# Kernel tuning notes

Hardware: AMD Instinct MI355X
Metric: run time of the kernel (lower is better)

## Reference

```python
import jax, jax.numpy as jnp
import numpy as np

B = 256                       # graphs in batch
NS = [4096, 2048, 1024, 512]  # nodes per graph at each stage (pool halves)
F_IN = 3                      # num_feature
D = 64                        # dim_cell
EPB = [32768, 16384, 8192]    # edges per graph at each layer (deg ~8)
NEG = 0.2                     # GATConv leaky_relu negative slope
EPS = 1e-5                    # BatchNorm eps
L = 3                         # layer_cell


def setup_inputs() -> dict:
    key = jax.random.key(0)
    ks = jax.random.split(key, 16)
    inp = {"x": jax.random.normal(ks[0], (B * NS[0], F_IN), jnp.float32)}
    dims = [F_IN, D, D]
    for i in range(L):
        inp[f"W{i}"] = jax.random.normal(ks[1 + i], (dims[i], D), jnp.float32) / np.sqrt(dims[i]).astype(np.float32)
        inp[f"as{i}"] = jax.random.normal(ks[4 + i], (D,), jnp.float32) * 0.1
        inp[f"ad{i}"] = jax.random.normal(ks[7 + i], (D,), jnp.float32) * 0.1
        inp[f"b{i}"] = jnp.zeros((D,), jnp.float32)
        inp[f"e{i}"] = jax.random.randint(ks[10 + i], (2, EPB[i]), 0, NS[i], jnp.int32)
        # cluster assignment: merge node pairs -> every cluster id occupied
        inp[f"c{i}"] = (jnp.arange(NS[i], dtype=jnp.int32) // 2)
    return inp


def _tile_edges(edge, n_per_graph):
    # replicate per-graph edge list across batch with node offsets, then add self-loops
    offs = (jnp.arange(B, dtype=edge.dtype) * n_per_graph)
    e = (edge[:, None, :] + offs[None, :, None]).reshape(2, -1)  # [2, B*E]
    loops = jnp.arange(B * n_per_graph, dtype=edge.dtype)
    return jnp.concatenate([e, jnp.stack([loops, loops])], axis=1)


def _gat(x, W, a_src, a_dst, bias, edge, n_tot):
    # PyG GATConv, heads=1: shared linear, edge-softmax over incoming edges
    h = x @ W                                # [n_tot, D]
    al_s = h @ a_src                         # [n_tot]
    al_d = h @ a_dst
    src, dst = edge[0], edge[1]              # message src j -> target i
    e = jax.nn.leaky_relu(al_s[src] + al_d[dst], NEG)
    m = jax.ops.segment_max(e, dst, num_segments=n_tot)
    ex = jnp.exp(e - m[dst])
    z = jax.ops.segment_sum(ex, dst, num_segments=n_tot)
    alpha = ex / z[dst]                      # softmax per target node
    out = jax.ops.segment_sum(alpha[:, None] * h[src], dst, num_segments=n_tot)
    return out + bias


def reference(x, W0, as0, ad0, b0, W1, as1, ad1, b1, W2, as2, ad2, b2,
              e0, e1, e2, c0, c1, c2):
    Ws, As, Ad, Bs = [W0, W1, W2], [as0, as1, as2], [ad0, ad1, ad2], [b0, b1, b2]
    Es, Cs = [e0, e1, e2], [c0, c1, c2]
    h = x
    for i in range(L):
        n_tot = B * NS[i]
        edge = _tile_edges(Es[i], NS[i])
        h = jax.nn.relu(_gat(h, Ws[i], As[i], Ad[i], Bs[i], edge, n_tot))
        # cluster max_pool: scatter-max nodes into clusters, offset per graph
        c_out = NS[i + 1]
        seg = (Cs[i][None, :] + (jnp.arange(B, dtype=jnp.int32) * c_out)[:, None]).reshape(-1)
        h = jax.ops.segment_max(h, seg, num_segments=B * c_out)
        # BatchNorm1d(affine=False), training-mode batch statistics
        h = (h - h.mean(axis=0)) * jax.lax.rsqrt(h.var(axis=0) + EPS)
    return h.reshape(B, NS[L] * D)
```

## Files before the change

### kernel.cpp

```cpp
#include <hip/hip_runtime.h>
#include <stdint.h>

#define NEG_SLOPE 0.2f
#define BN_EPS 1e-5f

typedef unsigned short u16;
typedef unsigned int   u32;
typedef __attribute__((ext_vector_type(2))) float  v2f;
typedef __attribute__((ext_vector_type(4))) float  f32x4;
typedef __attribute__((ext_vector_type(8))) short  short8;

__device__ __forceinline__ float lrelu(float x){ return fmaxf(x, NEG_SLOPE*x); }
__device__ __forceinline__ float bf2f(u16 u){ return __uint_as_float(((u32)u) << 16); }
__device__ __forceinline__ u16 f2bf(float f){
  u32 u = __float_as_uint(f);
  return (u16)((u + 0x7fffu + ((u >> 16) & 1u)) >> 16);
}

__global__ __launch_bounds__(256) void init_k(int* __restrict__ counts, u32* __restrict__ s0,
                                              u32* __restrict__ s1, u32* __restrict__ s2,
                                              int nc, int n0, int n1, int n2){
  int t = blockIdx.x*256 + threadIdx.x;
  int y = blockIdx.y;
  if (y==0){ if (t<nc) counts[t]=0; }
  else {
    u32* sd = (y==1)?s0:(y==2)?s1:s2;
    int n   = (y==1)?n0:(y==2)?n1:n2;
    if (t<n) sd[t]=0xFFFFFFFFu;
  }
}

__global__ __launch_bounds__(256) void hist_all_k(const int* __restrict__ el0, const int* __restrict__ el1,
                                                  const int* __restrict__ el2, int* __restrict__ c0,
                                                  int* __restrict__ c1, int* __restrict__ c2,
                                                  int n0, int n1, int n2){
  int t = blockIdx.x*256 + threadIdx.x;
  int L = blockIdx.y;
  const int* dst = (L==0)?(el0+n0):(L==1)?(el1+n1):(el2+n2);
  int* counts    = (L==0)?c0:(L==1)?c1:c2;
  int n          = (L==0)?n0:(L==1)?n1:n2;
  if (t < n) atomicAdd(&counts[dst[t]], 1);
}

__global__ __launch_bounds__(1024) void scan_all_k(int* __restrict__ c0, int* __restrict__ c1, int* __restrict__ c2,
                         int* __restrict__ ip0, int* __restrict__ ip1, int* __restrict__ ip2,
                         int* __restrict__ cu0, int* __restrict__ cu1, int* __restrict__ cu2,
                         u32* __restrict__ sd0, u32* __restrict__ sd1, u32* __restrict__ sd2,
                         int n0, int n1, int n2){
  int L = blockIdx.x;
  const int* counts = (L==0)?c0:(L==1)?c1:c2;
  int* indptr2      = (L==0)?ip0:(L==1)?ip1:ip2;
  int* cursor       = (L==0)?cu0:(L==1)?cu1:cu2;
  u32* sd           = (L==0)?sd0:(L==1)?sd1:sd2;
  int n             = (L==0)?n0:(L==1)?n1:n2;
  __shared__ int part[1024];
  int tid = threadIdx.x;
  int base = tid*4;
  int v0=0,v1=0,v2=0,v3=0;
  if (base+0<n) v0 = (counts[base+0]+4)&~3;
  if (base+1<n) v1 = (counts[base+1]+4)&~3;
  if (base+2<n) v2 = (counts[base+2]+4)&~3;
  if (base+3<n) v3 = (counts[base+3]+4)&~3;
  part[tid] = v0+v1+v2+v3;
  __syncthreads();
  for (int off=1; off<1024; off<<=1){
    int t2 = (tid>=off)?part[tid-off]:0;
    __syncthreads();
    part[tid] += t2;
    __syncthreads();
  }
  int run = (tid>0)?part[tid-1]:0;
  if (base+0<n){ indptr2[base+0]=run; cursor[base+0]=run+1; sd[run]=(u32)(base+0)|((u32)(base+0)<<16); run+=v0; }
  if (base+1<n){ indptr2[base+1]=run; cursor[base+1]=run+1; sd[run]=(u32)(base+1)|((u32)(base+1)<<16); run+=v1; }
  if (base+2<n){ indptr2[base+2]=run; cursor[base+2]=run+1; sd[run]=(u32)(base+2)|((u32)(base+2)<<16); run+=v2; }
  if (base+3<n){ indptr2[base+3]=run; cursor[base+3]=run+1; sd[run]=(u32)(base+3)|((u32)(base+3)<<16); run+=v3; }
  if (tid==0) indptr2[n] = part[1023];
}

__global__ __launch_bounds__(256) void scatter_all_k(const int* __restrict__ el0, const int* __restrict__ el1,
                         const int* __restrict__ el2, int* __restrict__ cu0, int* __restrict__ cu1,
                         int* __restrict__ cu2, u32* __restrict__ sd0, u32* __restrict__ sd1,
                         u32* __restrict__ sd2, int n0, int n1, int n2){
  int t = blockIdx.x*256 + threadIdx.x;
  int L = blockIdx.y;
  const int* el = (L==0)?el0:(L==1)?el1:el2;
  int* cursor   = (L==0)?cu0:(L==1)?cu1:cu2;
  u32* sd       = (L==0)?sd0:(L==1)?sd1:sd2;
  int n         = (L==0)?n0:(L==1)?n1:n2;
  if (t < n){
    int dd = el[n + t];
    int p = atomicAdd(&cursor[dd], 1);
    sd[p] = (u32)el[t] | ((u32)dd << 16);
  }
}

__global__ __launch_bounds__(1024) void pairsort_k(const int* __restrict__ c0, const int* __restrict__ c1,
                         const int* __restrict__ c2, u16* __restrict__ pm0, u16* __restrict__ pm1,
                         u16* __restrict__ pm2, int np0, int np1, int np2){
  int L = blockIdx.x;
  const int* counts = (L==0)?c0:(L==1)?c1:c2;
  u16* perm = (L==0)?pm0:(L==1)?pm1:pm2;
  int np    = (L==0)?np0:(L==1)?np1:np2;
  __shared__ int hist[64];
  __shared__ int pos[64];
  int t = threadIdx.x;
  if (t < 64) hist[t] = 0;
  __syncthreads();
  for (int p=t; p<np; p+=1024){
    int k = min(max(counts[2*p], counts[2*p+1]), 63);
    atomicAdd(&hist[k], 1);
  }
  __syncthreads();
  if (t == 0){ int run=0; for (int i=0;i<64;i++){ pos[i]=run; run+=hist[i]; } }
  __syncthreads();
  for (int p=t; p<np; p+=1024){
    int k = min(max(counts[2*p], counts[2*p+1]), 63);
    int q = atomicAdd(&pos[k], 1);
    perm[q] = (u16)p;
  }
}

__global__ __launch_bounds__(256) void gemm3_k(const float* __restrict__ x, const float* __restrict__ Wg,
                        const float* __restrict__ asrc, const float* __restrict__ adst,
                        u16* __restrict__ h, float* __restrict__ als, float* __restrict__ ald, int nrows8)
{
  const int l = threadIdx.x & 63;
  const int g = l >> 3;
  const int o = l & 7;
  float W0[8], W1[8], W2[8];
  float vs0=0.f,vs1=0.f,vs2=0.f,vd0=0.f,vd1=0.f,vd2=0.f;
  #pragma unroll
  for (int j=0;j<8;j++){
    W0[j] = Wg[      o*8 + j];
    W1[j] = Wg[ 64 + o*8 + j];
    W2[j] = Wg[128 + o*8 + j];
    float as = asrc[o*8 + j], ad = adst[o*8 + j];
    vs0 = fmaf(W0[j], as, vs0); vs1 = fmaf(W1[j], as, vs1); vs2 = fmaf(W2[j], as, vs2);
    vd0 = fmaf(W0[j], ad, vd0); vd1 = fmaf(W1[j], ad, vd1); vd2 = fmaf(W2[j], ad, vd2);
  }
  #pragma unroll
  for (int off=1; off<8; off<<=1){
    vs0 += __shfl_xor(vs0,off); vs1 += __shfl_xor(vs1,off); vs2 += __shfl_xor(vs2,off);
    vd0 += __shfl_xor(vd0,off); vd1 += __shfl_xor(vd1,off); vd2 += __shfl_xor(vd2,off);
  }
  int wv = blockIdx.x*4 + (int)(threadIdx.x>>6);
  int stride = gridDim.x*4;
  for (int blk = wv; blk < nrows8; blk += stride){
    int r = blk*8 + g;
    float x0 = x[(size_t)r*3+0];
    float x1 = x[(size_t)r*3+1];
    float x2 = x[(size_t)r*3+2];
    u32 pk[4];
    #pragma unroll
    for (int j=0;j<8;j+=2){
      float a0 = fmaf(x0, W0[j],   fmaf(x1, W1[j],   x2*W2[j]));
      float a1 = fmaf(x0, W0[j+1], fmaf(x1, W1[j+1], x2*W2[j+1]));
      pk[j>>1] = (u32)f2bf(a0) | ((u32)f2bf(a1) << 16);
    }
    ((int4*)(h + ((size_t)r << 6)))[o] = make_int4((int)pk[0],(int)pk[1],(int)pk[2],(int)pk[3]);
    if (o == 0){
      als[r] = fmaf(x2, vs2, fmaf(x1, vs1, x0*vs0));
      ald[r] = fmaf(x2, vd2, fmaf(x1, vd1, x0*vd0));
    }
  }
}

__global__ __launch_bounds__(128) void prep_w_k(const float* __restrict__ W, const float* __restrict__ asrc,
                        const float* __restrict__ adst, const float* __restrict__ scratch, float invN,
                        u16* __restrict__ wswz, float* __restrict__ cvec){
  __shared__ float mean_s[64], rstd_s[64], vs_s[64], vd_s[64], cv_s[64], acc[128];
  int t = threadIdx.x;
  float s = 0.f;
  #pragma unroll 8
  for (int b2=0;b2<256;b2++) s += scratch[b2*128 + t];
  acc[t] = s;
  __syncthreads();
  if (t < 64){
    float m = acc[t]*invN;
    float var = acc[64+t]*invN - m*m;
    mean_s[t] = m; rstd_s[t] = rsqrtf(var + BN_EPS);
  }
  __syncthreads();
  if (t < 64){
    float c = 0.f;
    for (int k=0;k<64;k++) c = fmaf(mean_s[k]*rstd_s[k], W[k*64+t], c);
    cv_s[t] = c; cvec[t] = c;
    float vs = 0.f, vd = 0.f;
    for (int col=0; col<64; col++){
      float wv = W[t*64+col];
      vs = fmaf(wv, asrc[col], vs);
      vd = fmaf(wv, adst[col], vd);
    }
    vs_s[t] = rstd_s[t]*vs; vd_s[t] = rstd_s[t]*vd;
  }
  __syncthreads();
  if (t == 0){
    float cs=0.f, cd=0.f;
    for (int col=0; col<64; col++){ cs = fmaf(cv_s[col], asrc[col], cs); cd = fmaf(cv_s[col], adst[col], cd); }
    cvec[64] = cs; cvec[65] = cd;
  }
  if (t < 64){
    #pragma unroll
    for (int f=0; f<8; f++){
      int tt = f >> 1, ch = f & 1;
      #pragma unroll
      for (int j=0; j<8; j++){
        int k   = ch*32 + (t>>4)*8 + j;
        int col = tt*16 + (t&15);
        wswz[(f*64 + t)*8 + j] = f2bf(rstd_s[k] * W[k*64 + col]);
      }
    }
    #pragma unroll
    for (int f=8; f<10; f++){
      int ch = f - 8;
      #pragma unroll
      for (int j=0; j<8; j++){
        int k = ch*32 + (t>>4)*8 + j;
        int colp = t & 15;
        float val = (colp==0)? vs_s[k] : (colp==1)? vd_s[k] : 0.f;
        wswz[(f*64 + t)*8 + j] = f2bf(val);
      }
    }
  }
}

__global__ __launch_bounds__(256) void gemm64_mfma_k(const u16* __restrict__ Pin, const u16* __restrict__ wswz,
                        const float* __restrict__ cvec,
                        u16* __restrict__ h, float* __restrict__ als, float* __restrict__ ald, int nblk16)
{
  const int l = threadIdx.x & 63;
  const int q = l >> 4;
  const int c = l & 15;
  short8 B[10];
  const int4* wsw = (const int4*)wswz;
  #pragma unroll
  for (int f=0; f<10; f++){
    int4 v = wsw[f*64 + l];
    B[f] = *(short8*)&v;
  }
  float cl[4];
  #pragma unroll
  for (int t=0;t<4;t++) cl[t] = cvec[t*16+c];
  const float const_s = cvec[64], const_d = cvec[65];
  int gw = blockIdx.x*4 + (int)(threadIdx.x>>6);
  int stride = gridDim.x*4;
  for (int blk = gw; blk < nblk16; blk += stride){
    size_t rowbase = (size_t)blk*16;
    const int4* arow = (const int4*)(Pin + (rowbase + c)*64);
    int4 a0v = arow[q];
    int4 a1v = arow[4+q];
    short8 A0 = *(short8*)&a0v, A1 = *(short8*)&a1v;
    f32x4 C0={0.f,0.f,0.f,0.f}, C1=C0, C2=C0, C3=C0, C4=C0;
    C0 = __builtin_amdgcn_mfma_f32_16x16x32_bf16(A0, B[0], C0, 0,0,0);
    C0 = __builtin_amdgcn_mfma_f32_16x16x32_bf16(A1, B[1], C0, 0,0,0);
    C1 = __builtin_amdgcn_mfma_f32_16x16x32_bf16(A0, B[2], C1, 0,0,0);
    C1 = __builtin_amdgcn_mfma_f32_16x16x32_bf16(A1, B[3], C1, 0,0,0);
    C2 = __builtin_amdgcn_mfma_f32_16x16x32_bf16(A0, B[4], C2, 0,0,0);
    C2 = __builtin_amdgcn_mfma_f32_16x16x32_bf16(A1, B[5], C2, 0,0,0);
    C3 = __builtin_amdgcn_mfma_f32_16x16x32_bf16(A0, B[6], C3, 0,0,0);
    C3 = __builtin_amdgcn_mfma_f32_16x16x32_bf16(A1, B[7], C3, 0,0,0);
    C4 = __builtin_amdgcn_mfma_f32_16x16x32_bf16(A0, B[8], C4, 0,0,0);
    C4 = __builtin_amdgcn_mfma_f32_16x16x32_bf16(A1, B[9], C4, 0,0,0);
    #pragma unroll
    for (int t=0;t<4;t++){
      f32x4 C = (t==0)?C0:(t==1)?C1:(t==2)?C2:C3;
      #pragma unroll
      for (int reg=0;reg<4;reg++){
        h[(rowbase + q*4 + reg)*64 + t*16 + c] = f2bf(C[reg] - cl[t]);
      }
    }
    if (c == 0){
      #pragma unroll
      for (int reg=0;reg<4;reg++) als[rowbase + q*4 + reg] = C4[reg] - const_s;
    } else if (c == 1){
      #pragma unroll
      for (int reg=0;reg<4;reg++) ald[rowbase + q*4 + reg] = C4[reg] - const_d;
    }
  }
}

__global__ __launch_bounds__(256) void wfill_k(const u32* __restrict__ ell_sd,
                        const float* __restrict__ als, const float* __restrict__ ald,
                        u32* __restrict__ epack, int cap, int log2NS)
{
  int slot = blockIdx.x*256 + threadIdx.x;
  int g = blockIdx.y;
  u32 v = ell_sd[slot];
  int nmask = (1<<log2NS)-1;
  int s = (int)(v & 0xffffu);
  int d = (int)(v >> 16);
  int base = g << log2NS;
  float e = als[base + (s & nmask)] + ald[base + (d & nmask)];
  u32 w = (v == 0xFFFFFFFFu) ? 0u : ((u32)f2bf(__expf(lrelu(e))) << 16);
  epack[(size_t)g*cap + slot] = (v & 0xffffu) | w;
}

__global__ __launch_bounds__(256) void gat_pool_k(const u16* __restrict__ h, const float* __restrict__ bias,
                      const int* __restrict__ indptr2, const int* __restrict__ counts,
                      const u16* __restrict__ perm, const u32* __restrict__ epack, u16* __restrict__ P,
                      int log2NS, int cap, int nwaves)
{
  const int l = threadIdx.x & 63;
  const int g = l >> 3;
  const int o = l & 7;
  const int NB  = gridDim.x;
  const int bid = blockIdx.x;
  const int lb  = (bid & 7) * (NB >> 3) + (bid >> 3);
  const int wv  = lb * 4 + (int)(threadIdx.x >> 6);
  if (wv >= nwaves) return;

  const int wbits = log2NS - 3;
  const int b    = wv >> wbits;
  const int widx = wv & ((1 << wbits) - 1);
  const int pairslot = widx*4 + (g >> 1);
  const int prow = perm[pairslot];
  const int d = 2*prow + (g & 1);
  const int nmask = (1 << log2NS) - 1;
  const u32* hb = (const u32*)(h + ((((size_t)b << log2NS)) << 6)) + (o << 2);
  const u32* erow = epack + (size_t)b * cap;

  const int p0  = indptr2[d];
  const int cnt = counts[d] + 1;

  const float* bp = bias + (o << 3);
  float4 bA = *(const float4*)(bp);
  float4 bB = *(const float4*)(bp + 4);

  v2f a01={0.f,0.f}, a23={0.f,0.f}, a45={0.f,0.f}, a67={0.f,0.f};
  float z = 0.f;

  u32 eA = erow[p0];
  int sA = (int)(eA & 0xffffu) & nmask;
  const u32* hpA = hb + ((size_t)sA << 5);
  u32 rA0=hpA[0], rA1=hpA[1], rA2=hpA[2], rA3=hpA[3];
  u32 eB = erow[p0 + 1];

  for (int it = 0; it < cnt; ++it){
    int sB = (int)(eB & 0xffffu) & nmask;
    const u32* hpB = hb + ((size_t)sB << 5);
    u32 rB0=hpB[0], rB1=hpB[1], rB2=hpB[2], rB3=hpB[3];
    u32 eC = erow[p0 + it + 2];
    float w = __uint_as_float(eA & 0xffff0000u);
    z += w;
    v2f w2 = {w, w};
    a01 += (v2f){ __uint_as_float(rA0 << 16), __uint_as_float(rA0 & 0xffff0000u) } * w2;
    a23 += (v2f){ __uint_as_float(rA1 << 16), __uint_as_float(rA1 & 0xffff0000u) } * w2;
    a45 += (v2f){ __uint_as_float(rA2 << 16), __uint_as_float(rA2 & 0xffff0000u) } * w2;
    a67 += (v2f){ __uint_as_float(rA3 << 16), __uint_as_float(rA3 & 0xffff0000u) } * w2;
    eA = eB; eB = eC;
    rA0 = rB0; rA1 = rB1; rA2 = rB2; rA3 = rB3;
  }

  float rz = __builtin_amdgcn_rcpf(z);
  float q0 = fmaxf(fmaf(a01.x, rz, bA.x), 0.f);
  float q1 = fmaxf(fmaf(a01.y, rz, bA.y), 0.f);
  float q2 = fmaxf(fmaf(a23.x, rz, bA.z), 0.f);
  float q3 = fmaxf(fmaf(a23.y, rz, bA.w), 0.f);
  float q4 = fmaxf(fmaf(a45.x, rz, bB.x), 0.f);
  float q5 = fmaxf(fmaf(a45.y, rz, bB.y), 0.f);
  float q6 = fmaxf(fmaf(a67.x, rz, bB.z), 0.f);
  float q7 = fmaxf(fmaf(a67.y, rz, bB.w), 0.f);
  q0 = fmaxf(q0, __shfl_xor(q0, 8));
  q1 = fmaxf(q1, __shfl_xor(q1, 8));
  q2 = fmaxf(q2, __shfl_xor(q2, 8));
  q3 = fmaxf(q3, __shfl_xor(q3, 8));
  q4 = fmaxf(q4, __shfl_xor(q4, 8));
  q5 = fmaxf(q5, __shfl_xor(q5, 8));
  q6 = fmaxf(q6, __shfl_xor(q6, 8));
  q7 = fmaxf(q7, __shfl_xor(q7, 8));
  if ((g & 1) == 0){
    u32 w0 = (u32)f2bf(q0) | ((u32)f2bf(q1) << 16);
    u32 w1 = (u32)f2bf(q2) | ((u32)f2bf(q3) << 16);
    u32 w2p = (u32)f2bf(q4) | ((u32)f2bf(q5) << 16);
    u32 w3 = (u32)f2bf(q6) | ((u32)f2bf(q7) << 16);
    size_t prowg = ((size_t)b << (log2NS - 1)) + prow;
    ((int4*)(P + (prowg << 6)))[o] = make_int4((int)w0,(int)w1,(int)w2p,(int)w3);
  }
}

__global__ __launch_bounds__(256) void bn_stats_k(const u16* __restrict__ P, float* __restrict__ scratch, int iters){
  const int l = threadIdx.x & 63;
  int gw = blockIdx.x*4 + (threadIdx.x>>6);
  int GW = gridDim.x*4;
  float s = 0.f, s2 = 0.f;
  #pragma unroll 4
  for (int i = 0; i < iters; i++){
    int r = gw + i*GW;
    float v = bf2f(P[(size_t)r*64 + l]);
    s += v; s2 = fmaf(v, v, s2);
  }
  __shared__ float ls[256], ls2[256];
  ls[threadIdx.x] = s; ls2[threadIdx.x] = s2;
  __syncthreads();
  if (threadIdx.x < 64){
    float S  = ls[threadIdx.x] + ls[threadIdx.x+64] + ls[threadIdx.x+128] + ls[threadIdx.x+192];
    float S2 = ls2[threadIdx.x] + ls2[threadIdx.x+64] + ls2[threadIdx.x+128] + ls2[threadIdx.x+192];
    scratch[blockIdx.x*128 + threadIdx.x] = S;
    scratch[blockIdx.x*128 + 64 + threadIdx.x] = S2;
  }
}

__global__ __launch_bounds__(128) void bn_finish_k(const float* __restrict__ scratch, float* __restrict__ stats,
                                                   int nblocks, float invN){
  __shared__ float accs[128];
  int j = threadIdx.x;
  float s = 0.f;
  #pragma unroll 8
  for (int b=0;b<nblocks;b++) s += scratch[b*128 + j];
  accs[j] = s;
  __syncthreads();
  if (j < 64){
    float m = accs[j]*invN;
    float var = accs[j+64]*invN - m*m;
    stats[j] = m;
    stats[64+j] = rsqrtf(var + BN_EPS);
  }
}

__global__ __launch_bounds__(256) void bn_apply_k(const u32* __restrict__ P2, const float* __restrict__ stats,
                                                  float4* __restrict__ out, int nq){
  int t = blockIdx.x*256 + threadIdx.x;
  if (t >= nq) return;
  int l = (t*4) & 63;
  u32 v0 = P2[t*2], v1 = P2[t*2+1];
  float4 r;
  r.x = (__uint_as_float((v0 & 0xffffu) << 16) - stats[l+0]) * stats[64+l+0];
  r.y = (__uint_as_float( v0 & 0xffff0000u    ) - stats[l+1]) * stats[64+l+1];
  r.z = (__uint_as_float((v1 & 0xffffu) << 16) - stats[l+2]) * stats[64+l+2];
  r.w = (__uint_as_float( v1 & 0xffff0000u    ) - stats[l+3]) * stats[64+l+3];
  out[t] = r;
}

extern "C" void kernel_launch(void* const* d_in, const int* in_sizes, int n_in,
                              void* d_out, int out_size, void* d_ws, size_t ws_size,
                              hipStream_t stream)
{
  const float* x      = (const float*)d_in[0];
  const float* Wl[3]  = {(const float*)d_in[1], (const float*)d_in[7],  (const float*)d_in[13]};
  const float* asl[3] = {(const float*)d_in[2], (const float*)d_in[8],  (const float*)d_in[14]};
  const float* adl[3] = {(const float*)d_in[3], (const float*)d_in[9],  (const float*)d_in[15]};
  const float* bl[3]  = {(const float*)d_in[4], (const float*)d_in[10], (const float*)d_in[16]};
  const int*   el[3]  = {(const int*)d_in[5],   (const int*)d_in[11],   (const int*)d_in[17]};

  const int NS[4]  = {4096, 2048, 1024, 512};
  const int EPB[3] = {32768, 16384, 8192};
  const int LOG2NS[3] = {12, 11, 10};
  const int ECAP[3] = {32768+4*4096, 16384+4*2048, 8192+4*1024};
  const int BATCH = 256;

  char* ws = (char*)d_ws;
  size_t off = 0;
  auto alloc = [&](size_t bytes)->char*{
    char* p = ws + off; off += (bytes + 255) & ~(size_t)255; return p;
  };

  u16*   hbuf    = (u16*)alloc((size_t)BATCH*NS[0]*64*2);
  u16*   Pbuf    = (u16*)alloc((size_t)BATCH*NS[1]*64*2);
  u32*   epack   = (u32*)alloc(((size_t)BATCH*ECAP[0] + 64)*4);
  float* als     = (float*)alloc((size_t)BATCH*NS[0]*4);
  float* ald     = (float*)alloc((size_t)BATCH*NS[0]*4);
  float* scratch = (float*)alloc(256*128*4);
  float* stats   = (float*)alloc(128*4);
  u16*   wswz    = (u16*)alloc(10*64*8*2);
  float* cvec    = (float*)alloc(128*4);
  int* counts_all = (int*)alloc((size_t)(NS[0]+NS[1]+NS[2])*4);
  int* cursor_all = (int*)alloc((size_t)(NS[0]+NS[1]+NS[2])*4);
  int *counts[3], *cursor[3], *indptr2[3];
  u32* ell_sd[3];
  u16* perm[3];
  counts[0]=counts_all; counts[1]=counts_all+NS[0]; counts[2]=counts_all+NS[0]+NS[1];
  cursor[0]=cursor_all; cursor[1]=cursor_all+NS[0]; cursor[2]=cursor_all+NS[0]+NS[1];
  for (int i=0;i<3;i++){
    indptr2[i] = (int*)alloc((size_t)(NS[i]+1)*4);
    ell_sd[i]  = (u32*)alloc((size_t)(ECAP[i]+16)*4);
    perm[i]    = (u16*)alloc((size_t)NS[i]);
  }
  if (off > ws_size) return;

  int ctot = NS[0]+NS[1]+NS[2];
  {
    dim3 ginit((ECAP[0]+16+255)/256, 4);
    init_k<<<ginit, 256, 0, stream>>>(counts_all, ell_sd[0], ell_sd[1], ell_sd[2],
                                      ctot, ECAP[0]+16, ECAP[1]+16, ECAP[2]+16);
    dim3 ghist(EPB[0]/256, 3);
    hist_all_k<<<ghist, 256, 0, stream>>>(el[0], el[1], el[2], counts[0], counts[1], counts[2],
                                          EPB[0], EPB[1], EPB[2]);
    scan_all_k<<<3, 1024, 0, stream>>>(counts[0], counts[1], counts[2],
                                       indptr2[0], indptr2[1], indptr2[2],
                                       cursor[0], cursor[1], cursor[2],
                                       ell_sd[0], ell_sd[1], ell_sd[2],
                                       NS[0], NS[1], NS[2]);
    scatter_all_k<<<ghist, 256, 0, stream>>>(el[0], el[1], el[2],
                                             cursor[0], cursor[1], cursor[2],
                                             ell_sd[0], ell_sd[1], ell_sd[2],
                                             EPB[0], EPB[1], EPB[2]);
    pairsort_k<<<3, 1024, 0, stream>>>(counts[0], counts[1], counts[2],
                                       perm[0], perm[1], perm[2],
                                       NS[0]/2, NS[1]/2, NS[2]/2);
  }

  for (int i=0;i<3;i++){
    int ntot = BATCH*NS[i];

    if (i==0){
      gemm3_k<<<1024, 256, 0, stream>>>(x, Wl[0], asl[0], adl[0], hbuf, als, ald, ntot/8);
    } else {
      float invN = 1.0f / (float)(BATCH*NS[i]);
      prep_w_k<<<1, 128, 0, stream>>>(Wl[i], asl[i], adl[i], scratch, invN, wswz, cvec);
      gemm64_mfma_k<<<2048, 256, 0, stream>>>(Pbuf, wswz, cvec, hbuf, als, ald, ntot/16);
    }

    dim3 wgrid(ECAP[i]/256, BATCH);
    wfill_k<<<wgrid, 256, 0, stream>>>(ell_sd[i], als, ald, epack, ECAP[i], LOG2NS[i]);

    int nwaves = ntot/8;
    gat_pool_k<<<nwaves/4, 256, 0, stream>>>(hbuf, bl[i], indptr2[i], counts[i], perm[i], epack,
                                             Pbuf, LOG2NS[i], ECAP[i], nwaves);

    bn_stats_k<<<256, 256, 0, stream>>>(Pbuf, scratch, (ntot/2)/1024);
  }

  bn_finish_k<<<1, 128, 0, stream>>>(scratch, stats, 256, 1.0f/(float)(BATCH*NS[3]));
  int nq = out_size/4;
  bn_apply_k<<<(nq+255)/256, 256, 0, stream>>>((const u32*)Pbuf, stats, (float4*)d_out, nq);
}
```

Measured before the change: 610.7 us.

## Fuse edge-weight computation into gather kernel and drop the per-batch edge buffer

Removes the wfill kernel, which wrote a packed source-index and bf16 attention weight for every edge slot of every graph into a large per-batch buffer. gat_pool_k now reads a shared u16 source-index list and computes exp(leaky_relu(als[src]+ald[dst])) inline. The ELL array shrinks from u32 to u16. The aim is to cut a large global write and re-read plus one launch per layer. In exchange there is an extra gather of als per edge, redundant exp work across the 8 lanes of a node group, and a deeper software prefetch.

```diff
diff --git a/kernel.cpp b/kernel.cpp
--- a/kernel.cpp
+++ b/kernel.cpp
@@ -17,16 +17,16 @@
   return (u16)((u + 0x7fffu + ((u >> 16) & 1u)) >> 16);
 }
 
-__global__ __launch_bounds__(256) void init_k(int* __restrict__ counts, u32* __restrict__ s0,
-                                              u32* __restrict__ s1, u32* __restrict__ s2,
+__global__ __launch_bounds__(256) void init_k(int* __restrict__ counts, u16* __restrict__ s0,
+                                              u16* __restrict__ s1, u16* __restrict__ s2,
                                               int nc, int n0, int n1, int n2){
   int t = blockIdx.x*256 + threadIdx.x;
   int y = blockIdx.y;
   if (y==0){ if (t<nc) counts[t]=0; }
   else {
-    u32* sd = (y==1)?s0:(y==2)?s1:s2;
+    u16* sd = (y==1)?s0:(y==2)?s1:s2;
     int n   = (y==1)?n0:(y==2)?n1:n2;
-    if (t<n) sd[t]=0xFFFFFFFFu;
+    if (t<n) sd[t]=0xFFFFu;
   }
 }
 
@@ -45,13 +45,13 @@
 __global__ __launch_bounds__(1024) void scan_all_k(int* __restrict__ c0, int* __restrict__ c1, int* __restrict__ c2,
                          int* __restrict__ ip0, int* __restrict__ ip1, int* __restrict__ ip2,
                          int* __restrict__ cu0, int* __restrict__ cu1, int* __restrict__ cu2,
-                         u32* __restrict__ sd0, u32* __restrict__ sd1, u32* __restrict__ sd2,
+                         u16* __restrict__ sd0, u16* __restrict__ sd1, u16* __restrict__ sd2,
                          int n0, int n1, int n2){
   int L = blockIdx.x;
   const int* counts = (L==0)?c0:(L==1)?c1:c2;
   int* indptr2      = (L==0)?ip0:(L==1)?ip1:ip2;
   int* cursor       = (L==0)?cu0:(L==1)?cu1:cu2;
-  u32* sd           = (L==0)?sd0:(L==1)?sd1:sd2;
+  u16* ell_src      = (L==0)?sd0:(L==1)?sd1:sd2;
   int n             = (L==0)?n0:(L==1)?n1:n2;
   __shared__ int part[1024];
   int tid = threadIdx.x;
@@ -70,27 +70,27 @@
     __syncthreads();
   }
   int run = (tid>0)?part[tid-1]:0;
-  if (base+0<n){ indptr2[base+0]=run; cursor[base+0]=run+1; sd[run]=(u32)(base+0)|((u32)(base+0)<<16); run+=v0; }
-  if (base+1<n){ indptr2[base+1]=run; cursor[base+1]=run+1; sd[run]=(u32)(base+1)|((u32)(base+1)<<16); run+=v1; }
-  if (base+2<n){ indptr2[base+2]=run; cursor[base+2]=run+1; sd[run]=(u32)(base+2)|((u32)(base+2)<<16); run+=v2; }
-  if (base+3<n){ indptr2[base+3]=run; cursor[base+3]=run+1; sd[run]=(u32)(base+3)|((u32)(base+3)<<16); run+=v3; }
+  if (base+0<n){ indptr2[base+0]=run; cursor[base+0]=run+1; ell_src[run]=(u16)(base+0); run+=v0; }
+  if (base+1<n){ indptr2[base+1]=run; cursor[base+1]=run+1; ell_src[run]=(u16)(base+1); run+=v1; }
+  if (base+2<n){ indptr2[base+2]=run; cursor[base+2]=run+1; ell_src[run]=(u16)(base+2); run+=v2; }
+  if (base+3<n){ indptr2[base+3]=run; cursor[base+3]=run+1; ell_src[run]=(u16)(base+3); run+=v3; }
   if (tid==0) indptr2[n] = part[1023];
 }
 
 __global__ __launch_bounds__(256) void scatter_all_k(const int* __restrict__ el0, const int* __restrict__ el1,
                          const int* __restrict__ el2, int* __restrict__ cu0, int* __restrict__ cu1,
-                         int* __restrict__ cu2, u32* __restrict__ sd0, u32* __restrict__ sd1,
-                         u32* __restrict__ sd2, int n0, int n1, int n2){
+                         int* __restrict__ cu2, u16* __restrict__ sd0, u16* __restrict__ sd1,
+                         u16* __restrict__ sd2, int n0, int n1, int n2){
   int t = blockIdx.x*256 + threadIdx.x;
   int L = blockIdx.y;
   const int* el = (L==0)?el0:(L==1)?el1:el2;
   int* cursor   = (L==0)?cu0:(L==1)?cu1:cu2;
-  u32* sd       = (L==0)?sd0:(L==1)?sd1:sd2;
+  u16* ell_src  = (L==0)?sd0:(L==1)?sd1:sd2;
   int n         = (L==0)?n0:(L==1)?n1:n2;
   if (t < n){
     int dd = el[n + t];
     int p = atomicAdd(&cursor[dd], 1);
-    sd[p] = (u32)el[t] | ((u32)dd << 16);
+    ell_src[p] = (u16)el[t];
   }
 }
 
@@ -279,26 +279,11 @@
   }
 }
 
-__global__ __launch_bounds__(256) void wfill_k(const u32* __restrict__ ell_sd,
-                        const float* __restrict__ als, const float* __restrict__ ald,
-                        u32* __restrict__ epack, int cap, int log2NS)
-{
-  int slot = blockIdx.x*256 + threadIdx.x;
-  int g = blockIdx.y;
-  u32 v = ell_sd[slot];
-  int nmask = (1<<log2NS)-1;
-  int s = (int)(v & 0xffffu);
-  int d = (int)(v >> 16);
-  int base = g << log2NS;
-  float e = als[base + (s & nmask)] + ald[base + (d & nmask)];
-  u32 w = (v == 0xFFFFFFFFu) ? 0u : ((u32)f2bf(__expf(lrelu(e))) << 16);
-  epack[(size_t)g*cap + slot] = (v & 0xffffu) | w;
-}
-
 __global__ __launch_bounds__(256) void gat_pool_k(const u16* __restrict__ h, const float* __restrict__ bias,
                       const int* __restrict__ indptr2, const int* __restrict__ counts,
-                      const u16* __restrict__ perm, const u32* __restrict__ epack, u16* __restrict__ P,
-                      int log2NS, int cap, int nwaves)
+                      const u16* __restrict__ perm, const u16* __restrict__ ell_src,
+                      const float* __restrict__ als, const float* __restrict__ ald,
+                      u16* __restrict__ P, int log2NS, int nwaves)
 {
   const int l = threadIdx.x & 63;
   const int g = l >> 3;
@@ -316,11 +301,13 @@
   const int prow = perm[pairslot];
   const int d = 2*prow + (g & 1);
   const int nmask = (1 << log2NS) - 1;
-  const u32* hb = (const u32*)(h + ((((size_t)b << log2NS)) << 6)) + (o << 2);
-  const u32* erow = epack + (size_t)b * cap;
+  const int base = b << log2NS;
+  const u32* hb = (const u32*)(h + ((size_t)base << 6)) + (o << 2);
+  const float* alsg = als + base;
 
   const int p0  = indptr2[d];
   const int cnt = counts[d] + 1;
+  const float ald_d = ald[base + d];
 
   const float* bp = bias + (o << 3);
   float4 bA = *(const float4*)(bp);
@@ -329,26 +316,34 @@
   v2f a01={0.f,0.f}, a23={0.f,0.f}, a45={0.f,0.f}, a67={0.f,0.f};
   float z = 0.f;
 
-  u32 eA = erow[p0];
-  int sA = (int)(eA & 0xffffu) & nmask;
-  const u32* hpA = hb + ((size_t)sA << 5);
-  u32 rA0=hpA[0], rA1=hpA[1], rA2=hpA[2], rA3=hpA[3];
-  u32 eB = erow[p0 + 1];
+  int m0 = ell_src[p0];
+  int m1 = ell_src[p0+1];
+  int m2 = ell_src[p0+2];
+  int s0i = m0 & nmask;
+  const u32* hp0 = hb + ((size_t)s0i << 5);
+  u32 h00=hp0[0], h01=hp0[1], h02=hp0[2], h03=hp0[3];
+  float al0 = alsg[s0i];
+  int s1i = m1 & nmask;
+  const u32* hp1 = hb + ((size_t)s1i << 5);
+  u32 h10=hp1[0], h11=hp1[1], h12=hp1[2], h13=hp1[3];
+  float al1 = alsg[s1i];
 
   for (int it = 0; it < cnt; ++it){
-    int sB = (int)(eB & 0xffffu) & nmask;
-    const u32* hpB = hb + ((size_t)sB << 5);
-    u32 rB0=hpB[0], rB1=hpB[1], rB2=hpB[2], rB3=hpB[3];
-    u32 eC = erow[p0 + it + 2];
-    float w = __uint_as_float(eA & 0xffff0000u);
+    int s2i = m2 & nmask;
+    const u32* hp2 = hb + ((size_t)s2i << 5);
+    u32 n0=hp2[0], n1=hp2[1], n2=hp2[2], n3=hp2[3];
+    float al2 = alsg[s2i];
+    int m3 = ell_src[p0 + it + 3];
+    float w = (m0 == 0xFFFF) ? 0.f : __expf(lrelu(al0 + ald_d));
     z += w;
     v2f w2 = {w, w};
-    a01 += (v2f){ __uint_as_float(rA0 << 16), __uint_as_float(rA0 & 0xffff0000u) } * w2;
-    a23 += (v2f){ __uint_as_float(rA1 << 16), __uint_as_float(rA1 & 0xffff0000u) } * w2;
-    a45 += (v2f){ __uint_as_float(rA2 << 16), __uint_as_float(rA2 & 0xffff0000u) } * w2;
-    a67 += (v2f){ __uint_as_float(rA3 << 16), __uint_as_float(rA3 & 0xffff0000u) } * w2;
-    eA = eB; eB = eC;
-    rA0 = rB0; rA1 = rB1; rA2 = rB2; rA3 = rB3;
+    a01 += (v2f){ __uint_as_float(h00 << 16), __uint_as_float(h00 & 0xffff0000u) } * w2;
+    a23 += (v2f){ __uint_as_float(h01 << 16), __uint_as_float(h01 & 0xffff0000u) } * w2;
+    a45 += (v2f){ __uint_as_float(h02 << 16), __uint_as_float(h02 & 0xffff0000u) } * w2;
+    a67 += (v2f){ __uint_as_float(h03 << 16), __uint_as_float(h03 & 0xffff0000u) } * w2;
+    m0 = m1; m1 = m2; m2 = m3;
+    h00=h10; h01=h11; h02=h12; h03=h13; al0 = al1;
+    h10=n0;  h11=n1;  h12=n2;  h13=n3;  al1 = al2;
   }
 
   float rz = __builtin_amdgcn_rcpf(z);
@@ -456,7 +451,6 @@
 
   u16*   hbuf    = (u16*)alloc((size_t)BATCH*NS[0]*64*2);
   u16*   Pbuf    = (u16*)alloc((size_t)BATCH*NS[1]*64*2);
-  u32*   epack   = (u32*)alloc(((size_t)BATCH*ECAP[0] + 64)*4);
   float* als     = (float*)alloc((size_t)BATCH*NS[0]*4);
   float* ald     = (float*)alloc((size_t)BATCH*NS[0]*4);
   float* scratch = (float*)alloc(256*128*4);
@@ -466,13 +460,13 @@
   int* counts_all = (int*)alloc((size_t)(NS[0]+NS[1]+NS[2])*4);
   int* cursor_all = (int*)alloc((size_t)(NS[0]+NS[1]+NS[2])*4);
   int *counts[3], *cursor[3], *indptr2[3];
-  u32* ell_sd[3];
+  u16* ell_src[3];
   u16* perm[3];
   counts[0]=counts_all; counts[1]=counts_all+NS[0]; counts[2]=counts_all+NS[0]+NS[1];
   cursor[0]=cursor_all; cursor[1]=cursor_all+NS[0]; cursor[2]=cursor_all+NS[0]+NS[1];
   for (int i=0;i<3;i++){
     indptr2[i] = (int*)alloc((size_t)(NS[i]+1)*4);
-    ell_sd[i]  = (u32*)alloc((size_t)(ECAP[i]+16)*4);
+    ell_src[i] = (u16*)alloc((size_t)(ECAP[i]+16)*2);
     perm[i]    = (u16*)alloc((size_t)NS[i]);
   }
   if (off > ws_size) return;
@@ -480,7 +474,7 @@
   int ctot = NS[0]+NS[1]+NS[2];
   {
     dim3 ginit((ECAP[0]+16+255)/256, 4);
-    init_k<<<ginit, 256, 0, stream>>>(counts_all, ell_sd[0], ell_sd[1], ell_sd[2],
+    init_k<<<ginit, 256, 0, stream>>>(counts_all, ell_src[0], ell_src[1], ell_src[2],
                                       ctot, ECAP[0]+16, ECAP[1]+16, ECAP[2]+16);
     dim3 ghist(EPB[0]/256, 3);
     hist_all_k<<<ghist, 256, 0, stream>>>(el[0], el[1], el[2], counts[0], counts[1], counts[2],
@@ -488,11 +482,11 @@
     scan_all_k<<<3, 1024, 0, stream>>>(counts[0], counts[1], counts[2],
                                        indptr2[0], indptr2[1], indptr2[2],
                                        cursor[0], cursor[1], cursor[2],
-                                       ell_sd[0], ell_sd[1], ell_sd[2],
+                                       ell_src[0], ell_src[1], ell_src[2],
                                        NS[0], NS[1], NS[2]);
     scatter_all_k<<<ghist, 256, 0, stream>>>(el[0], el[1], el[2],
                                              cursor[0], cursor[1], cursor[2],
-                                             ell_sd[0], ell_sd[1], ell_sd[2],
+                                             ell_src[0], ell_src[1], ell_src[2],
                                              EPB[0], EPB[1], EPB[2]);
     pairsort_k<<<3, 1024, 0, stream>>>(counts[0], counts[1], counts[2],
                                        perm[0], perm[1], perm[2],
@@ -510,12 +504,10 @@
       gemm64_mfma_k<<<2048, 256, 0, stream>>>(Pbuf, wswz, cvec, hbuf, als, ald, ntot/16);
     }
 
-    dim3 wgrid(ECAP[i]/256, BATCH);
-    wfill_k<<<wgrid, 256, 0, stream>>>(ell_sd[i], als, ald, epack, ECAP[i], LOG2NS[i]);
-
     int nwaves = ntot/8;
-    gat_pool_k<<<nwaves/4, 256, 0, stream>>>(hbuf, bl[i], indptr2[i], counts[i], perm[i], epack,
-                                             Pbuf, LOG2NS[i], ECAP[i], nwaves);
+    gat_pool_k<<<nwaves/4, 256, 0, stream>>>(hbuf, bl[i], indptr2[i], counts[i], perm[i],
+                                             ell_src[i], als, ald,
+                                             Pbuf, LOG2NS[i], nwaves);
 
     bn_stats_k<<<256, 256, 0, stream>>>(Pbuf, scratch, (ntot/2)/1024);
   }
```

After: 550.9 us. 9.8% less time.
